# Kernel optimization log

Measured on AMD Instinct MI355X. Metric: run time of the kernel, lower is better.

## Reference

```python
import jax, jax.numpy as jnp
import numpy as np

B, T, C, H, D = 4, 2048, 1024, 16, 64
EPS = 1e-5

def setup_inputs() -> dict:
    key = jax.random.key(0)
    ks = jax.random.split(key, 8)
    s = lambda fan_in: 1.0 / np.sqrt(fan_in)
    return {
        'x': jax.random.normal(ks[0], (B, T, C), jnp.float32),
        'wq': jax.random.normal(ks[1], (H, C, D), jnp.float32) * s(C),
        'wk': jax.random.normal(ks[2], (H, C, D), jnp.float32) * s(C),
        'wv': jax.random.normal(ks[3], (H, C, D), jnp.float32) * s(C),
        'w_proj': jax.random.normal(ks[4], (C, C), jnp.float32) * s(C),
        'b_proj': jnp.zeros((C,), jnp.float32),
        'w1': jax.random.normal(ks[5], (C, 4 * C), jnp.float32) * s(C),
        'b1': jnp.zeros((4 * C,), jnp.float32),
        'w2': jax.random.normal(ks[6], (4 * C, C), jnp.float32) * s(4 * C),
        'b2': jnp.zeros((C,), jnp.float32),
        'g1': jnp.ones((C,), jnp.float32),
        'be1': jnp.zeros((C,), jnp.float32),
        'g2': jnp.ones((C,), jnp.float32),
        'be2': jnp.zeros((C,), jnp.float32),
    }

def layer_norm(x, g, b):
    mu = jnp.mean(x, axis=-1, keepdims=True)
    var = jnp.mean(jnp.square(x - mu), axis=-1, keepdims=True)
    return (x - mu) * jax.lax.rsqrt(var + EPS) * g + b

def reference(x, wq, wk, wv, w_proj, b_proj, w1, b1, w2, b2, g1, be1, g2, be2):
    # --- attention (pre-LN) ---
    xn = layer_norm(x, g1, be1)
    q = jnp.einsum('btc,hcd->bhtd', xn, wq)
    k = jnp.einsum('btc,hcd->bhtd', xn, wk)
    v = jnp.einsum('btc,hcd->bhtd', xn, wv)
    # NOTE: original scales by full embedding dim C (not head size)
    scores = jnp.einsum('bhtd,bhsd->bhts', q, k) * (C ** -0.5)
    causal = jnp.tril(jnp.ones((T, T), bool))
    scores = jnp.where(causal, scores, -jnp.inf)
    wei = jax.nn.softmax(scores, axis=-1)
    attn = jnp.einsum('bhts,bhsd->bhtd', wei, v)
    attn = attn.transpose(0, 2, 1, 3).reshape(B, T, C)  # concat heads
    x = x + attn @ w_proj + b_proj
    # --- FFN (pre-LN) ---
    xn2 = layer_norm(x, g2, be2)
    h = jax.nn.relu(xn2 @ w1 + b1)
    x = x + h @ w2 + b2
    return x
```

## Files before the change

kernel.cpp:

```cpp
#include <hip/hip_runtime.h>
#include <hip/hip_bf16.h>

#define B_ 4
#define T_ 2048
#define C_ 1024
#define H_ 16
#define D_ 64
#define M_ (B_*T_)

typedef unsigned short ushort;
typedef __attribute__((ext_vector_type(8))) short short8;
typedef __attribute__((ext_vector_type(8))) unsigned short ushort8;
typedef __attribute__((ext_vector_type(4))) float floatx4;
typedef __attribute__((ext_vector_type(4))) unsigned int uintx4;

static __device__ __forceinline__ float bf2f(ushort u) {
    unsigned int x = ((unsigned int)u) << 16;
    return __builtin_bit_cast(float, x);
}
static __device__ __forceinline__ ushort f2bf(float f) {
    unsigned int x = __builtin_bit_cast(unsigned int, f);
    unsigned int r = (x + 0x7fffu + ((x >> 16) & 1u)) >> 16;
    return (ushort)r;
}

typedef const __attribute__((address_space(1))) unsigned int gu32;
typedef __attribute__((address_space(3))) unsigned int lu32;
static __device__ __forceinline__ void glds16(const void* g, void* l) {
    __builtin_amdgcn_global_load_lds((gu32*)g, (lu32*)l, 16, 0, 0);
}

__global__ __launch_bounds__(256) void ln_kernel(
    const float* __restrict__ x, const float* __restrict__ g,
    const float* __restrict__ be, ushort* __restrict__ out)
{
    int row = blockIdx.x;
    int tid = threadIdx.x;
    const float* xr = x + (size_t)row * C_;
    float v[4];
    float s = 0.f, s2 = 0.f;
#pragma unroll
    for (int i = 0; i < 4; i++) {
        float t = xr[tid + i * 256];
        v[i] = t; s += t; s2 += t * t;
    }
#pragma unroll
    for (int off = 32; off; off >>= 1) {
        s  += __shfl_down(s, off);
        s2 += __shfl_down(s2, off);
    }
    __shared__ float rs[4], rs2[4];
    __shared__ float smu, srstd;
    int w = tid >> 6;
    if ((tid & 63) == 0) { rs[w] = s; rs2[w] = s2; }
    __syncthreads();
    if (tid == 0) {
        float ts  = rs[0] + rs[1] + rs[2] + rs[3];
        float ts2 = rs2[0] + rs2[1] + rs2[2] + rs2[3];
        float mu  = ts * (1.f / C_);
        float var = ts2 * (1.f / C_) - mu * mu;
        smu = mu; srstd = rsqrtf(var + 1e-5f);
    }
    __syncthreads();
    float mu = smu, r = srstd;
#pragma unroll
    for (int i = 0; i < 4; i++) {
        int c = tid + i * 256;
        out[(size_t)row * C_ + c] = f2bf((v[i] - mu) * r * g[c] + be[c]);
    }
}

__global__ __launch_bounds__(256) void transpose_conv(
    const float* __restrict__ in, ushort* __restrict__ out,
    int R, int Cn, long long in_bstride, long long out_bstride)
{
    __shared__ float tile[32][33];
    const float* ip = in + (size_t)blockIdx.z * in_bstride;
    ushort* op = out + (size_t)blockIdx.z * out_bstride;
    int tx = threadIdx.x;
    int ty = threadIdx.y;
    int c0 = blockIdx.x * 32, r0 = blockIdx.y * 32;
#pragma unroll
    for (int i = 0; i < 32; i += 8) {
        tile[ty + i][tx] = ip[(size_t)(r0 + ty + i) * Cn + c0 + tx];
    }
    __syncthreads();
#pragma unroll
    for (int i = 0; i < 32; i += 8) {
        int oc = c0 + ty + i;
        int orr = r0 + tx;
        op[(size_t)oc * R + orr] = f2bf(tile[tx][ty + i]);
    }
}

__global__ __launch_bounds__(256) void vtrans_kernel(
    const ushort* __restrict__ qkv, ushort* __restrict__ VtG)
{
    int bh = blockIdx.y;
    int b = bh >> 4, h = bh & 15;
    int j0 = blockIdx.x * 64;
    int tid = threadIdx.x;
    __shared__ unsigned int X[64 * 33];
    const ushort* Vg = qkv + (size_t)(b * T_) * 3072 + 2048 + h * 64;
#pragma unroll
    for (int it = 0; it < 2; it++) {
        int j = (tid >> 3) + it * 32;
        int dp = (tid & 7) * 4;
        uintx4 val = *(const uintx4*)(Vg + (size_t)(j0 + j) * 3072 + dp * 2);
#pragma unroll
        for (int k = 0; k < 4; k++) X[j * 33 + dp + k] = val[k];
    }
    __syncthreads();
    int dp = tid >> 3, jc = tid & 7;
    unsigned int v[8];
#pragma unroll
    for (int jj = 0; jj < 8; jj++) v[jj] = X[(jc * 8 + jj) * 33 + dp];
    ushort8 lo, hi;
#pragma unroll
    for (int jj = 0; jj < 8; jj++) {
        lo[jj] = (ushort)(v[jj] & 0xffffu);
        hi[jj] = (ushort)(v[jj] >> 16);
    }
    size_t r0 = ((size_t)(h * 256 + 4 * (2 * dp) + b)) * T_ + j0 + jc * 8;
    size_t r1 = ((size_t)(h * 256 + 4 * (2 * dp + 1) + b)) * T_ + j0 + jc * 8;
    *(ushort8*)&VtG[r0] = lo;
    *(ushort8*)&VtG[r1] = hi;
}

template<int BN, bool OUTBF16, bool BIAS, bool RELU, bool RESID>
__global__ __launch_bounds__(512, 2) void gemm256_kernel(
    const ushort* __restrict__ A,
    const ushort* __restrict__ Bt,
    const float* __restrict__ bias,
    const float* __restrict__ resid,
    void* __restrict__ Cout,
    int Mdim, int Ndim, int K)
{
    constexpr int WN   = (BN == 256) ? 4 : 2;
    constexpr int MI   = 2 * WN;
    constexpr int NI   = 4;
    constexpr int BISS = BN / 64;

    __shared__ ushort As[2][256 * 64];
    __shared__ ushort Bs[2][BN * 64];

    int gridX = gridDim.x;
    int nwg = gridX * gridDim.y;
    int bid = blockIdx.y * gridX + blockIdx.x;
    int cpx = nwg >> 3;
    int swz = (bid & 7) * cpx + (bid >> 3);
    int bx = swz % gridX, by = swz / gridX;
    int m0 = by * 256, n0 = bx * BN;

    int tid = threadIdx.x;
    int wave = tid >> 6, lane = tid & 63;
    int quad = lane >> 4, l16 = lane & 15;
    int wr = wave / WN, wc = wave % WN;
    int wm = wr * (MI * 16);
    int wn = wc * 64;

    int lrow = lane >> 3;
    int lchunk = (lane & 7) ^ (lrow & 7);

    floatx4 acc[MI][NI] = {};

    int nt = K >> 6;

    auto stage = [&](int t, int sbuf) {
        int k0 = t << 6;
#pragma unroll
        for (int it = 0; it < 4; it++) {
            int rb = it * 64 + wave * 8;
            glds16(A + (size_t)(m0 + rb + lrow) * K + k0 + lchunk * 8, &As[sbuf][rb * 64]);
        }
#pragma unroll
        for (int it = 0; it < BISS; it++) {
            int rb = it * 64 + wave * 8;
            glds16(Bt + (size_t)(n0 + rb + lrow) * K + k0 + lchunk * 8, &Bs[sbuf][rb * 64]);
        }
    };

    stage(0, 0);
    stage(1, 1);
    if constexpr (BN == 256) asm volatile("s_waitcnt vmcnt(8)" ::: "memory");
    else                     asm volatile("s_waitcnt vmcnt(6)" ::: "memory");
    __builtin_amdgcn_s_barrier();
    asm volatile("" ::: "memory");

    int buf = 0;
    for (int t = 0; t < nt; ++t) {
        short8 af[MI], bfv[NI];
#pragma unroll
        for (int mi = 0; mi < MI; mi++)
            af[mi] = *(const short8*)&As[buf][(wm + mi * 16 + l16) * 64 + ((quad ^ (l16 & 7)) * 8)];
#pragma unroll
        for (int ni = 0; ni < NI; ni++)
            bfv[ni] = *(const short8*)&Bs[buf][(wn + ni * 16 + l16) * 64 + ((quad ^ (l16 & 7)) * 8)];
        __builtin_amdgcn_s_setprio(1);
#pragma unroll
        for (int mi = 0; mi < MI; mi++)
#pragma unroll
            for (int ni = 0; ni < NI; ni++)
                acc[mi][ni] = __builtin_amdgcn_mfma_f32_16x16x32_bf16(af[mi], bfv[ni], acc[mi][ni], 0, 0, 0);
        __builtin_amdgcn_s_setprio(0);

        short8 ag[MI], bg[NI];
#pragma unroll
        for (int mi = 0; mi < MI; mi++)
            ag[mi] = *(const short8*)&As[buf][(wm + mi * 16 + l16) * 64 + (((4 + quad) ^ (l16 & 7)) * 8)];
#pragma unroll
        for (int ni = 0; ni < NI; ni++)
            bg[ni] = *(const short8*)&Bs[buf][(wn + ni * 16 + l16) * 64 + (((4 + quad) ^ (l16 & 7)) * 8)];
        asm volatile("s_waitcnt lgkmcnt(0)" ::: "memory");
        __builtin_amdgcn_s_barrier();
        asm volatile("" ::: "memory");
        if (t + 2 < nt) stage(t + 2, buf);

        __builtin_amdgcn_s_setprio(1);
#pragma unroll
        for (int mi = 0; mi < MI; mi++)
#pragma unroll
            for (int ni = 0; ni < NI; ni++)
                acc[mi][ni] = __builtin_amdgcn_mfma_f32_16x16x32_bf16(ag[mi], bg[ni], acc[mi][ni], 0, 0, 0);
        __builtin_amdgcn_s_setprio(0);

        if (t + 2 < nt) {
            if constexpr (BN == 256) asm volatile("s_waitcnt vmcnt(8)" ::: "memory");
            else                     asm volatile("s_waitcnt vmcnt(6)" ::: "memory");
        } else {
            asm volatile("s_waitcnt vmcnt(0)" ::: "memory");
        }
        __builtin_amdgcn_s_barrier();
        asm volatile("" ::: "memory");
        buf ^= 1;
    }

    int r4 = quad * 4;
#pragma unroll
    for (int mi = 0; mi < MI; mi++) {
#pragma unroll
        for (int ni = 0; ni < NI; ni++) {
#pragma unroll
            for (int r = 0; r < 4; r++) {
                int gm = m0 + wm + mi * 16 + r4 + r;
                int gn = n0 + wn + ni * 16 + l16;
                float v = acc[mi][ni][r];
                if (BIAS)  v += bias[gn];
                if (RESID) v += resid[(size_t)gm * Ndim + gn];
                if (RELU)  v = fmaxf(v, 0.f);
                if (OUTBF16) ((ushort*)Cout)[(size_t)gm * Ndim + gn] = f2bf(v);
                else         ((float*)Cout)[(size_t)gm * Ndim + gn] = v;
            }
        }
    }
}

__global__ __launch_bounds__(256, 2) void attn_kernel(
    const ushort* __restrict__ qkv,
    const ushort* __restrict__ VtG,
    ushort* __restrict__ attnb)
{
    const int LD = 3072;
    int bid = blockIdx.x;
    int bh = (bid & 7) * 8 + ((bid >> 3) & 7);
    int qt = 15 - (bid >> 6);
    int b = bh >> 4, h = bh & 15;
    int t0 = qt * 128;
    int tid = threadIdx.x;
    int wave = tid >> 6, lane = tid & 63;
    int quad = lane >> 4, l16 = lane & 15;

    __shared__ ushort Ks[2][64 * 64];
    __shared__ ushort Vt[2][64 * 64];
    __shared__ ushort Ps[4][32 * 72];

    const ushort* Qg = qkv + (size_t)(b * T_) * LD + h * 64;
    const ushort* Kg = Qg + 1024;
    const ushort* VtB = VtG + (size_t)(h * 256 + b) * T_;

    int qrow_base = t0 + wave * 32;
    int lrow = lane >> 3;
    int lchunk = (lane & 7) ^ (lrow & 7);

    short8 qa[2][2];
#pragma unroll
    for (int mt = 0; mt < 2; mt++) {
        const ushort* qp = Qg + (size_t)(qrow_base + mt * 16 + l16) * LD + quad * 8;
        ushort8 q0 = *(const ushort8*)qp;
        ushort8 q1 = *(const ushort8*)(qp + 32);
        ushort8 a0, a1;
#pragma unroll
        for (int d = 0; d < 8; d++) {
            a0[d] = f2bf(bf2f(q0[d]) * 0.03125f);
            a1[d] = f2bf(bf2f(q1[d]) * 0.03125f);
        }
        qa[mt][0] = __builtin_bit_cast(short8, a0);
        qa[mt][1] = __builtin_bit_cast(short8, a1);
    }

    float l_part[2][4];
    floatx4 o_acc[2][4];
#pragma unroll
    for (int mt = 0; mt < 2; mt++)
#pragma unroll
        for (int r = 0; r < 4; r++) {
            l_part[mt][r] = 0.f;
            o_acc[mt][r] = floatx4{0.f, 0.f, 0.f, 0.f};
        }

    int nIter = t0 / 64 + 2;

#pragma unroll
    for (int it = 0; it < 2; it++) {
        int rb = (wave * 2 + it) * 8;
        int r = rb + lrow;
        glds16(Kg  + (size_t)r * LD + lchunk * 8, &Ks[0][rb * 64]);
        glds16(VtB + (size_t)r * (4 * T_) + lchunk * 8, &Vt[0][rb * 64]);
    }

    for (int ii = 0; ii < nIter; ii++) {
        int s0 = ii * 64;
        int buf = ii & 1;
        __syncthreads();
        if (ii + 1 < nIter) {
            int sn = s0 + 64;
#pragma unroll
            for (int it = 0; it < 2; it++) {
                int rb = (wave * 2 + it) * 8;
                int r = rb + lrow;
                glds16(Kg  + (size_t)(sn + r) * LD + lchunk * 8, &Ks[buf ^ 1][rb * 64]);
                glds16(VtB + (size_t)r * (4 * T_) + sn + lchunk * 8, &Vt[buf ^ 1][rb * 64]);
            }
        }

        if (s0 <= qrow_base + 31) {
#pragma unroll
            for (int mt = 0; mt < 2; mt++) {
                floatx4 s_acc[4];
#pragma unroll
                for (int nt = 0; nt < 4; nt++) {
                    int krow = nt * 16 + l16;
                    const short8* kb0 = (const short8*)&Ks[buf][krow * 64 + ((quad       ^ (l16 & 7)) * 8)];
                    const short8* kb1 = (const short8*)&Ks[buf][krow * 64 + (((4 + quad) ^ (l16 & 7)) * 8)];
                    floatx4 z = {0.f, 0.f, 0.f, 0.f};
                    z = __builtin_amdgcn_mfma_f32_16x16x32_bf16(qa[mt][0], *kb0, z, 0, 0, 0);
                    s_acc[nt] = __builtin_amdgcn_mfma_f32_16x16x32_bf16(qa[mt][1], *kb1, z, 0, 0, 0);
                }
                int base_mt = qrow_base + mt * 16;
                if (s0 + 63 > base_mt) {
#pragma unroll
                    for (int nt = 0; nt < 4; nt++)
#pragma unroll
                        for (int r = 0; r < 4; r++) {
                            int gi = base_mt + quad * 4 + r;
                            int gj = s0 + nt * 16 + l16;
                            if (gj > gi) s_acc[nt][r] = -INFINITY;
                        }
                }
#pragma unroll
                for (int nt = 0; nt < 4; nt++)
#pragma unroll
                    for (int r = 0; r < 4; r++) {
                        float e = __expf(s_acc[nt][r]);
                        s_acc[nt][r] = e;
                        l_part[mt][r] += e;
                        Ps[wave][(mt * 16 + quad * 4 + r) * 72 + nt * 16 + l16] = f2bf(e);
                    }
            }
            asm volatile("s_waitcnt lgkmcnt(0)" ::: "memory");
            short8 pa[2][2];
#pragma unroll
            for (int mt = 0; mt < 2; mt++) {
                pa[mt][0] = *(const short8*)&Ps[wave][(mt * 16 + l16) * 72 + quad * 8];
                pa[mt][1] = *(const short8*)&Ps[wave][(mt * 16 + l16) * 72 + quad * 8 + 32];
            }
#pragma unroll
            for (int dt = 0; dt < 4; dt++) {
                int vrow = dt * 16 + l16;
                const short8* vb0 = (const short8*)&Vt[buf][vrow * 64 + ((quad       ^ (l16 & 7)) * 8)];
                const short8* vb1 = (const short8*)&Vt[buf][vrow * 64 + (((4 + quad) ^ (l16 & 7)) * 8)];
#pragma unroll
                for (int mt = 0; mt < 2; mt++) {
                    o_acc[mt][dt] = __builtin_amdgcn_mfma_f32_16x16x32_bf16(pa[mt][0], *vb0, o_acc[mt][dt], 0, 0, 0);
                    o_acc[mt][dt] = __builtin_amdgcn_mfma_f32_16x16x32_bf16(pa[mt][1], *vb1, o_acc[mt][dt], 0, 0, 0);
                }
            }
        }
    }

#pragma unroll
    for (int mt = 0; mt < 2; mt++)
#pragma unroll
        for (int r = 0; r < 4; r++) {
            float ls = l_part[mt][r];
            ls += __shfl_xor(ls, 1);
            ls += __shfl_xor(ls, 2);
            ls += __shfl_xor(ls, 4);
            ls += __shfl_xor(ls, 8);
            float inv = 1.f / ls;
            int gi = qrow_base + mt * 16 + quad * 4 + r;
            ushort* op = attnb + (size_t)(b * T_ + gi) * 1024 + h * 64;
#pragma unroll
            for (int dt = 0; dt < 4; dt++)
                op[dt * 16 + l16] = f2bf(o_acc[mt][dt][r] * inv);
        }
}

extern "C" void kernel_launch(void* const* d_in, const int* in_sizes, int n_in,
                              void* d_out, int out_size, void* d_ws, size_t ws_size,
                              hipStream_t stream) {
    (void)in_sizes; (void)n_in; (void)out_size; (void)ws_size;
    const float* x      = (const float*)d_in[0];
    const float* wq     = (const float*)d_in[1];
    const float* wk     = (const float*)d_in[2];
    const float* wv     = (const float*)d_in[3];
    const float* w_proj = (const float*)d_in[4];
    const float* b_proj = (const float*)d_in[5];
    const float* w1     = (const float*)d_in[6];
    const float* b1     = (const float*)d_in[7];
    const float* w2     = (const float*)d_in[8];
    const float* b2     = (const float*)d_in[9];
    const float* g1     = (const float*)d_in[10];
    const float* be1    = (const float*)d_in[11];
    const float* g2     = (const float*)d_in[12];
    const float* be2    = (const float*)d_in[13];
    float* out = (float*)d_out;

    char* ws = (char*)d_ws;
    const size_t MB = 1024ull * 1024ull;
    ushort* xn     = (ushort*)(ws + 0);
    ushort* qkv    = (ushort*)(ws + 16 * MB);
    ushort* attnb  = (ushort*)(ws + 64 * MB);
    ushort* hbuf   = (ushort*)(ws + 16 * MB);
    float*  x1     = (float*) (ws + 80 * MB);
    ushort* VtG    = (ushort*)(ws + 80 * MB);
    ushort* WqkvT  = (ushort*)(ws + 112 * MB);
    ushort* WprojT = (ushort*)(ws + 118 * MB);
    ushort* W1T    = (ushort*)(ws + 120 * MB);
    ushort* W2T    = (ushort*)(ws + 128 * MB);
    ushort* xn2 = xn;

    dim3 tb(32, 8);
    ln_kernel<<<M_, 256, 0, stream>>>(x, g1, be1, xn);
    transpose_conv<<<dim3(D_ / 32, C_ / 32, H_), tb, 0, stream>>>(wq, WqkvT,               C_, D_, (long long)C_ * D_, (long long)D_ * C_);
    transpose_conv<<<dim3(D_ / 32, C_ / 32, H_), tb, 0, stream>>>(wk, WqkvT + C_ * C_,     C_, D_, (long long)C_ * D_, (long long)D_ * C_);
    transpose_conv<<<dim3(D_ / 32, C_ / 32, H_), tb, 0, stream>>>(wv, WqkvT + 2 * C_ * C_, C_, D_, (long long)C_ * D_, (long long)D_ * C_);
    transpose_conv<<<dim3(C_ / 32, C_ / 32, 1), tb, 0, stream>>>(w_proj, WprojT, C_, C_, 0, 0);
    transpose_conv<<<dim3(4 * C_ / 32, C_ / 32, 1), tb, 0, stream>>>(w1, W1T, C_, 4 * C_, 0, 0);
    transpose_conv<<<dim3(C_ / 32, 4 * C_ / 32, 1), tb, 0, stream>>>(w2, W2T, 4 * C_, C_, 0, 0);
    gemm256_kernel<128, true, false, false, false><<<dim3(3072 / 128, M_ / 256), 512, 0, stream>>>(
        xn, WqkvT, nullptr, nullptr, qkv, M_, 3072, C_);
    vtrans_kernel<<<dim3(T_ / 64, B_ * H_), 256, 0, stream>>>(qkv, VtG);
    attn_kernel<<<1024, 256, 0, stream>>>(qkv, VtG, attnb);
    gemm256_kernel<128, false, true, false, true><<<dim3(C_ / 128, M_ / 256), 512, 0, stream>>>(
        attnb, WprojT, b_proj, x, x1, M_, C_, C_);
    ln_kernel<<<M_, 256, 0, stream>>>(x1, g2, be2, xn2);
    gemm256_kernel<256, true, true, true, false><<<dim3(4 * C_ / 256, M_ / 256), 512, 0, stream>>>(
        xn2, W1T, b1, nullptr, hbuf, M_, 4 * C_, C_);
    gemm256_kernel<128, false, true, false, true><<<dim3(C_ / 128, M_ / 256), 512, 0, stream>>>(
        hbuf, W2T, b2, x1, out, M_, C_, 4 * C_);
}
```

Measured before the change: 467.1 us.

## Interleave LDS fragment reads with MFMA quarters in GEMM main loop

Splits each K-tile's MFMA work into four half-M by half-K groups and loads the next group's A/B fragments from LDS while the current group computes. The first fragments of the next tile are read right after the barrier, and the final MFMA group runs after the next global-to-LDS stage is issued. The aim is to hide LDS read latency and keep the matrix units busy across the barrier. In exchange it needs more live fragment registers and a more intricate schedule, which could hurt occupancy at 512 threads with two blocks per CU.

```diff
diff --git a/kernel.cpp b/kernel.cpp
--- a/kernel.cpp
+++ b/kernel.cpp
@@ -136,10 +136,12 @@
     void* __restrict__ Cout,
     int Mdim, int Ndim, int K)
 {
-    constexpr int WN   = (BN == 256) ? 4 : 2;
-    constexpr int MI   = 2 * WN;
-    constexpr int NI   = 4;
+    constexpr int WN  = (BN == 256) ? 4 : 2;
+    constexpr int MI  = 2 * WN;
+    constexpr int MH  = MI / 2;
+    constexpr int NI  = 4;
     constexpr int BISS = BN / 64;
+    constexpr int LPS  = 4 + BISS;
 
     __shared__ ushort As[2][256 * 64];
     __shared__ ushort Bs[2][BN * 64];
@@ -163,7 +165,6 @@
     int lchunk = (lane & 7) ^ (lrow & 7);
 
     floatx4 acc[MI][NI] = {};
-
     int nt = K >> 6;
 
     auto stage = [&](int t, int sbuf) {
@@ -180,59 +181,73 @@
         }
     };
 
+    auto rdA = [&](short8* dst, int buf, int kk, int mh) {
+#pragma unroll
+        for (int i = 0; i < MH; i++) {
+            int r = wm + (mh * MH + i) * 16 + l16;
+            dst[i] = *(const short8*)&As[buf][r * 64 + (((kk * 4 + quad) ^ (r & 7)) * 8)];
+        }
+    };
+    auto rdB = [&](short8* dst, int buf, int kk) {
+#pragma unroll
+        for (int n = 0; n < NI; n++) {
+            int r = wn + n * 16 + l16;
+            dst[n] = *(const short8*)&Bs[buf][r * 64 + (((kk * 4 + quad) ^ (r & 7)) * 8)];
+        }
+    };
+    auto mm = [&](const short8* a, const short8* b, int mh) {
+        __builtin_amdgcn_s_setprio(1);
+#pragma unroll
+        for (int i = 0; i < MH; i++)
+#pragma unroll
+            for (int n = 0; n < NI; n++)
+                acc[mh * MH + i][n] =
+                    __builtin_amdgcn_mfma_f32_16x16x32_bf16(a[i], b[n], acc[mh * MH + i][n], 0, 0, 0);
+        __builtin_amdgcn_s_setprio(0);
+    };
+
     stage(0, 0);
     stage(1, 1);
-    if constexpr (BN == 256) asm volatile("s_waitcnt vmcnt(8)" ::: "memory");
-    else                     asm volatile("s_waitcnt vmcnt(6)" ::: "memory");
+    asm volatile("s_waitcnt vmcnt(%0)" :: "i"(LPS) : "memory");
     __builtin_amdgcn_s_barrier();
     asm volatile("" ::: "memory");
 
-    int buf = 0;
+    short8 bf0[NI], bf1[NI];
+    short8 aP[MH], aQ[MH];
+
+    rdB(bf0, 0, 0);
+    rdA(aP, 0, 0, 0);
+
     for (int t = 0; t < nt; ++t) {
-        short8 af[MI], bfv[NI];
-#pragma unroll
-        for (int mi = 0; mi < MI; mi++)
-            af[mi] = *(const short8*)&As[buf][(wm + mi * 16 + l16) * 64 + ((quad ^ (l16 & 7)) * 8)];
-#pragma unroll
-        for (int ni = 0; ni < NI; ni++)
-            bfv[ni] = *(const short8*)&Bs[buf][(wn + ni * 16 + l16) * 64 + ((quad ^ (l16 & 7)) * 8)];
-        __builtin_amdgcn_s_setprio(1);
-#pragma unroll
-        for (int mi = 0; mi < MI; mi++)
-#pragma unroll
-            for (int ni = 0; ni < NI; ni++)
-                acc[mi][ni] = __builtin_amdgcn_mfma_f32_16x16x32_bf16(af[mi], bfv[ni], acc[mi][ni], 0, 0, 0);
-        __builtin_amdgcn_s_setprio(0);
-
-        short8 ag[MI], bg[NI];
-#pragma unroll
-        for (int mi = 0; mi < MI; mi++)
-            ag[mi] = *(const short8*)&As[buf][(wm + mi * 16 + l16) * 64 + (((4 + quad) ^ (l16 & 7)) * 8)];
-#pragma unroll
-        for (int ni = 0; ni < NI; ni++)
-            bg[ni] = *(const short8*)&Bs[buf][(wn + ni * 16 + l16) * 64 + (((4 + quad) ^ (l16 & 7)) * 8)];
+        int buf = t & 1;
+
+        rdA(aQ, buf, 0, 1);
+        mm(aP, bf0, 0);
+
+        rdB(bf1, buf, 1);
+        rdA(aP, buf, 1, 0);
+        mm(aQ, bf0, 1);
+
+        rdA(aQ, buf, 1, 1);
+        mm(aP, bf1, 0);
+
         asm volatile("s_waitcnt lgkmcnt(0)" ::: "memory");
         __builtin_amdgcn_s_barrier();
         asm volatile("" ::: "memory");
-        if (t + 2 < nt) stage(t + 2, buf);
-
-        __builtin_amdgcn_s_setprio(1);
-#pragma unroll
-        for (int mi = 0; mi < MI; mi++)
-#pragma unroll
-            for (int ni = 0; ni < NI; ni++)
-                acc[mi][ni] = __builtin_amdgcn_mfma_f32_16x16x32_bf16(ag[mi], bg[ni], acc[mi][ni], 0, 0, 0);
-        __builtin_amdgcn_s_setprio(0);
-
         if (t + 2 < nt) {
-            if constexpr (BN == 256) asm volatile("s_waitcnt vmcnt(8)" ::: "memory");
-            else                     asm volatile("s_waitcnt vmcnt(6)" ::: "memory");
+            stage(t + 2, buf);
+            asm volatile("s_waitcnt vmcnt(%0)" :: "i"(LPS) : "memory");
         } else {
             asm volatile("s_waitcnt vmcnt(0)" ::: "memory");
         }
         __builtin_amdgcn_s_barrier();
         asm volatile("" ::: "memory");
-        buf ^= 1;
+
+        if (t + 1 < nt) {
+            rdB(bf0, buf ^ 1, 0);
+            rdA(aP, buf ^ 1, 0, 0);
+        }
+        mm(aQ, bf1, 1);
     }
 
     int r4 = quad * 4;
```

Result: slower. 495.7 us (+6.1%).

## Add 256x256 GEMM with quarter-staged pipelined loads for QKV and FFN1

Applied to the files above, without the earlier changes.

Introduces a new 256x256-tile GEMM kernel that splits A and B tiles into 128-row halves and interleaves global-to-LDS loads with four MFMA quarters per k-step, with grouped block swizzling for L2 reuse. It replaces the old kernel for the QKV projection and the first FFN GEMM. The old GEMM's inner loop is also restructured into a kk loop with a generalized swizzle index. The aim is finer overlap of memory traffic and matrix math plus larger tiles. The cost is many more barriers and tight hand-tuned vmcnt counts that are easy to get wrong.

```diff
diff --git a/kernel.cpp b/kernel.cpp
--- a/kernel.cpp
+++ b/kernel.cpp
@@ -125,6 +125,154 @@
     size_t r1 = ((size_t)(h * 256 + 4 * (2 * dp + 1) + b)) * T_ + j0 + jc * 8;
     *(ushort8*)&VtG[r0] = lo;
     *(ushort8*)&VtG[r1] = hi;
+}
+
+template<bool OUTBF16, bool BIAS, bool RELU, bool RESID>
+__global__ __launch_bounds__(512, 2) void gemm8p_kernel(
+    const ushort* __restrict__ A,
+    const ushort* __restrict__ Bt,
+    const float* __restrict__ bias,
+    const float* __restrict__ resid,
+    void* __restrict__ Cout,
+    int Mdim, int Ndim, int K)
+{
+    __shared__ ushort AL[2][2][128 * 64];
+    __shared__ ushort BL[2][2][128 * 64];
+
+    int gridX = gridDim.x;
+    int nwg = gridX * gridDim.y;
+    int bid = blockIdx.y * gridX + blockIdx.x;
+    int cpx = nwg >> 3;
+    int swz = (bid & 7) * cpx + (bid >> 3);
+    int bx = swz % gridX, by = swz / gridX;
+    int m0 = by * 256, n0 = bx * 256;
+
+    int tid = threadIdx.x;
+    int wave = tid >> 6, lane = tid & 63;
+    int quad = lane >> 4, l16 = lane & 15;
+    int wr = wave >> 2, wc = wave & 3;
+    int lrow = lane >> 3;
+    int lchunk = (lane & 7) ^ (lrow & 7);
+
+    int nt = K >> 6;
+
+    auto stA = [&](int t, int b, int h) {
+        if (t >= nt) t = nt - 1;
+#pragma unroll
+        for (int it = 0; it < 2; it++) {
+            int rb = it * 64 + wave * 8;
+            glds16(A + (size_t)(m0 + h * 128 + rb + lrow) * K + (t << 6) + lchunk * 8,
+                   &AL[b][h][rb * 64]);
+        }
+    };
+    auto stB = [&](int t, int b, int h) {
+        if (t >= nt) t = nt - 1;
+#pragma unroll
+        for (int it = 0; it < 2; it++) {
+            int rb = it * 64 + wave * 8;
+            glds16(Bt + (size_t)(n0 + h * 128 + rb + lrow) * K + (t << 6) + lchunk * 8,
+                   &BL[b][h][rb * 64]);
+        }
+    };
+
+    floatx4 acc[8][4] = {};
+    short8 Bf[4][2];
+    short8 Af[2][2];
+
+    auto rdB = [&](int b) {
+#pragma unroll
+        for (int n = 0; n < 4; n++) {
+            int nr = wc * 64 + n * 16 + l16;
+            int h = nr >> 7, r = nr & 127;
+#pragma unroll
+            for (int kk = 0; kk < 2; kk++)
+                Bf[n][kk] = *(const short8*)&BL[b][h][r * 64 + (((kk * 4 + quad) ^ (r & 7)) * 8)];
+        }
+    };
+    auto rdA = [&](int b, int q) {
+#pragma unroll
+        for (int mi = 0; mi < 2; mi++) {
+            int R = q * 64 + wr * 32 + mi * 16 + l16;
+            int h = R >> 7, r = R & 127;
+#pragma unroll
+            for (int kk = 0; kk < 2; kk++)
+                Af[mi][kk] = *(const short8*)&AL[b][h][r * 64 + (((kk * 4 + quad) ^ (r & 7)) * 8)];
+        }
+    };
+    auto mmq = [&](int q) {
+        __builtin_amdgcn_s_setprio(1);
+#pragma unroll
+        for (int kk = 0; kk < 2; kk++)
+#pragma unroll
+            for (int mi = 0; mi < 2; mi++)
+#pragma unroll
+                for (int n = 0; n < 4; n++)
+                    acc[q * 2 + mi][n] = __builtin_amdgcn_mfma_f32_16x16x32_bf16(
+                        Af[mi][kk], Bf[n][kk], acc[q * 2 + mi][n], 0, 0, 0);
+        __builtin_amdgcn_s_setprio(0);
+    };
+
+    stB(0, 0, 0); stB(0, 0, 1); stA(0, 0, 0); stA(0, 0, 1);
+    stB(1, 1, 0); stB(1, 1, 1); stA(1, 1, 0);
+    asm volatile("s_waitcnt vmcnt(8)" ::: "memory");
+    __builtin_amdgcn_s_barrier();
+
+    int J = nt >> 1;
+    for (int j = 0; j < J; j++) {
+        int ta = 2 * j, tb = 2 * j + 1;
+#pragma unroll
+        for (int hf = 0; hf < 2; hf++) {
+            rdB(hf); rdA(hf, 0);
+            if (hf == 0) stA(tb, 1, 1); else stA(ta + 2, 0, 1);
+            __builtin_amdgcn_s_barrier();
+            asm volatile("s_waitcnt lgkmcnt(0)" ::: "memory");
+            __builtin_amdgcn_sched_barrier(0);
+            mmq(0);
+            __builtin_amdgcn_s_barrier();
+            rdA(hf, 1);
+            if (hf == 0) stB(ta + 2, 0, 0); else stB(tb + 2, 1, 0);
+            __builtin_amdgcn_s_barrier();
+            asm volatile("s_waitcnt lgkmcnt(0)" ::: "memory");
+            __builtin_amdgcn_sched_barrier(0);
+            mmq(1);
+            asm volatile("s_waitcnt vmcnt(10)" ::: "memory");
+            __builtin_amdgcn_s_barrier();
+            rdA(hf, 2);
+            if (hf == 0) stB(ta + 2, 0, 1); else stB(tb + 2, 1, 1);
+            __builtin_amdgcn_s_barrier();
+            asm volatile("s_waitcnt lgkmcnt(0)" ::: "memory");
+            __builtin_amdgcn_sched_barrier(0);
+            mmq(2);
+            __builtin_amdgcn_s_barrier();
+            rdA(hf, 3);
+            if (hf == 0) stA(ta + 2, 0, 0); else stA(tb + 2, 1, 0);
+            __builtin_amdgcn_s_barrier();
+            asm volatile("s_waitcnt lgkmcnt(0)" ::: "memory");
+            __builtin_amdgcn_sched_barrier(0);
+            mmq(3);
+            asm volatile("s_waitcnt vmcnt(8)" ::: "memory");
+            __builtin_amdgcn_s_barrier();
+        }
+    }
+
+#pragma unroll
+    for (int am = 0; am < 8; am++) {
+        int q = am >> 1, mi = am & 1;
+#pragma unroll
+        for (int n = 0; n < 4; n++) {
+#pragma unroll
+            for (int r = 0; r < 4; r++) {
+                int gm = m0 + q * 64 + wr * 32 + mi * 16 + quad * 4 + r;
+                int gn = n0 + wc * 64 + n * 16 + l16;
+                float v = acc[am][n][r];
+                if (BIAS)  v += bias[gn];
+                if (RESID) v += resid[(size_t)gm * Ndim + gn];
+                if (RELU)  v = fmaxf(v, 0.f);
+                if (OUTBF16) ((ushort*)Cout)[(size_t)gm * Ndim + gn] = f2bf(v);
+                else         ((float*)Cout)[(size_t)gm * Ndim + gn] = v;
+            }
+        }
+    }
 }
 
 template<int BN, bool OUTBF16, bool BIAS, bool RELU, bool RESID>
@@ -189,41 +337,34 @@
 
     int buf = 0;
     for (int t = 0; t < nt; ++t) {
-        short8 af[MI], bfv[NI];
-#pragma unroll
-        for (int mi = 0; mi < MI; mi++)
-            af[mi] = *(const short8*)&As[buf][(wm + mi * 16 + l16) * 64 + ((quad ^ (l16 & 7)) * 8)];
-#pragma unroll
-        for (int ni = 0; ni < NI; ni++)
-            bfv[ni] = *(const short8*)&Bs[buf][(wn + ni * 16 + l16) * 64 + ((quad ^ (l16 & 7)) * 8)];
-        __builtin_amdgcn_s_setprio(1);
-#pragma unroll
-        for (int mi = 0; mi < MI; mi++)
-#pragma unroll
-            for (int ni = 0; ni < NI; ni++)
-                acc[mi][ni] = __builtin_amdgcn_mfma_f32_16x16x32_bf16(af[mi], bfv[ni], acc[mi][ni], 0, 0, 0);
-        __builtin_amdgcn_s_setprio(0);
-
-        short8 ag[MI], bg[NI];
-#pragma unroll
-        for (int mi = 0; mi < MI; mi++)
-            ag[mi] = *(const short8*)&As[buf][(wm + mi * 16 + l16) * 64 + (((4 + quad) ^ (l16 & 7)) * 8)];
-#pragma unroll
-        for (int ni = 0; ni < NI; ni++)
-            bg[ni] = *(const short8*)&Bs[buf][(wn + ni * 16 + l16) * 64 + (((4 + quad) ^ (l16 & 7)) * 8)];
-        asm volatile("s_waitcnt lgkmcnt(0)" ::: "memory");
-        __builtin_amdgcn_s_barrier();
-        asm volatile("" ::: "memory");
-        if (t + 2 < nt) stage(t + 2, buf);
-
-        __builtin_amdgcn_s_setprio(1);
-#pragma unroll
-        for (int mi = 0; mi < MI; mi++)
-#pragma unroll
-            for (int ni = 0; ni < NI; ni++)
-                acc[mi][ni] = __builtin_amdgcn_mfma_f32_16x16x32_bf16(ag[mi], bg[ni], acc[mi][ni], 0, 0, 0);
-        __builtin_amdgcn_s_setprio(0);
-
+#pragma unroll
+        for (int kk = 0; kk < 2; kk++) {
+            short8 af[MI], bfv[NI];
+            int c = kk * 4 + quad;
+#pragma unroll
+            for (int mi = 0; mi < MI; mi++) {
+                int r = wm + mi * 16 + l16;
+                af[mi] = *(const short8*)&As[buf][r * 64 + ((c ^ (r & 7)) * 8)];
+            }
+#pragma unroll
+            for (int ni = 0; ni < NI; ni++) {
+                int r = wn + ni * 16 + l16;
+                bfv[ni] = *(const short8*)&Bs[buf][r * 64 + ((c ^ (r & 7)) * 8)];
+            }
+            if (kk == 1) {
+                asm volatile("s_waitcnt lgkmcnt(0)" ::: "memory");
+                __builtin_amdgcn_s_barrier();
+                asm volatile("" ::: "memory");
+                if (t + 2 < nt) stage(t + 2, buf);
+            }
+            __builtin_amdgcn_s_setprio(1);
+#pragma unroll
+            for (int mi = 0; mi < MI; mi++)
+#pragma unroll
+                for (int ni = 0; ni < NI; ni++)
+                    acc[mi][ni] = __builtin_amdgcn_mfma_f32_16x16x32_bf16(af[mi], bfv[ni], acc[mi][ni], 0, 0, 0);
+            __builtin_amdgcn_s_setprio(0);
+        }
         if (t + 2 < nt) {
             if constexpr (BN == 256) asm volatile("s_waitcnt vmcnt(8)" ::: "memory");
             else                     asm volatile("s_waitcnt vmcnt(6)" ::: "memory");
@@ -448,14 +589,14 @@
     transpose_conv<<<dim3(C_ / 32, C_ / 32, 1), tb, 0, stream>>>(w_proj, WprojT, C_, C_, 0, 0);
     transpose_conv<<<dim3(4 * C_ / 32, C_ / 32, 1), tb, 0, stream>>>(w1, W1T, C_, 4 * C_, 0, 0);
     transpose_conv<<<dim3(C_ / 32, 4 * C_ / 32, 1), tb, 0, stream>>>(w2, W2T, 4 * C_, C_, 0, 0);
-    gemm256_kernel<128, true, false, false, false><<<dim3(3072 / 128, M_ / 256), 512, 0, stream>>>(
+    gemm8p_kernel<true, false, false, false><<<dim3(3072 / 256, M_ / 256), 512, 0, stream>>>(
         xn, WqkvT, nullptr, nullptr, qkv, M_, 3072, C_);
     vtrans_kernel<<<dim3(T_ / 64, B_ * H_), 256, 0, stream>>>(qkv, VtG);
     attn_kernel<<<1024, 256, 0, stream>>>(qkv, VtG, attnb);
     gemm256_kernel<128, false, true, false, true><<<dim3(C_ / 128, M_ / 256), 512, 0, stream>>>(
         attnb, WprojT, b_proj, x, x1, M_, C_, C_);
     ln_kernel<<<M_, 256, 0, stream>>>(x1, g2, be2, xn2);
-    gemm256_kernel<256, true, true, true, false><<<dim3(4 * C_ / 256, M_ / 256), 512, 0, stream>>>(
+    gemm8p_kernel<true, true, true, false><<<dim3(4 * C_ / 256, M_ / 256), 512, 0, stream>>>(
         xn2, W1T, b1, nullptr, hbuf, M_, 4 * C_, C_);
     gemm256_kernel<128, false, true, false, true><<<dim3(C_ / 128, M_ / 256), 512, 0, stream>>>(
         hbuf, W2T, b2, x1, out, M_, C_, 4 * C_);
```

Measured after the change: 467.5 us. No clear change (+0.1%).
